# Optimization experiments

Hardware: AMD Instinct MI355X
Metric: run time of the kernel (lower is better)

Reference implementation:

```python
import jax, jax.numpy as jnp
import numpy as np


def _deg2_idx(cpg):
    # pairs (c1, c2) with c1 <= c2, c2 inner loop -> matches torch nested loop order
    i, j = np.triu_indices(cpg)
    return i, j


def _deg3_idx(cpg):
    # triples (c1, c2, c3) with c1 <= c2 <= c3, same nesting order as torch loops
    t = np.array([(a, b, c) for a in range(cpg) for b in range(a, cpg) for c in range(b, cpg)], dtype=np.int32)
    return t[:, 0], t[:, 1], t[:, 2]


def setup_inputs() -> dict:
    key = jax.random.key(0)
    ks = jax.random.split(key, 7)
    B, C, H, W = 16, 256, 56, 56
    G = 32
    cpg = C // G  # 8
    n2 = cpg * (cpg + 1) // 2  # 36
    n3 = sum((i + 1) * (i + 2) // 2 for i in range(cpg))  # 120
    x = jax.random.normal(ks[0], (B, C, H, W), dtype=jnp.float32)
    w1 = jax.random.normal(ks[1], (G, cpg, cpg), dtype=jnp.float32) * 0.1
    b1 = jax.random.normal(ks[2], (G, cpg), dtype=jnp.float32) * 0.1
    w2 = jax.random.normal(ks[3], (G, cpg, n2), dtype=jnp.float32) * 0.1
    b2 = jax.random.normal(ks[4], (G, cpg), dtype=jnp.float32) * 0.1
    w3 = jax.random.normal(ks[5], (G, cpg, n3), dtype=jnp.float32) * 0.1
    b3 = jax.random.normal(ks[6], (G, cpg), dtype=jnp.float32) * 0.1
    return {"x": x, "w1": w1, "b1": b1, "w2": w2, "b2": b2, "w3": w3, "b3": b3}


def reference(x, w1, b1, w2, b2, w3, b3):
    B, C, H, W = x.shape
    G, cpg, _ = w1.shape
    xg = x.reshape(B, G, cpg, H, W)  # [B, G, cpg, H, W]

    i2, j2 = _deg2_idx(cpg)
    a3, b3i, c3 = _deg3_idx(cpg)

    # polynomial feature expansion (per group, vectorized over all dims)
    d2 = xg[:, :, i2] * xg[:, :, j2]                        # [B, G, n2, H, W]
    d3 = xg[:, :, a3] * xg[:, :, b3i] * xg[:, :, c3]        # [B, G, n3, H, W]

    # grouped 1x1 convs as per-group matmuls, summed (matches output += conv(...))
    out = jnp.einsum('bgkhw,gok->bgohw', xg, w1) + b1[None, :, :, None, None]
    out = out + jnp.einsum('bgkhw,gok->bgohw', d2, w2) + b2[None, :, :, None, None]
    out = out + jnp.einsum('bgkhw,gok->bgohw', d3, w3) + b3[None, :, :, None, None]
    return out.reshape(B, C, H, W)
```

## Files before the change

kernel.cpp:

```cpp
#include <hip/hip_runtime.h>

#define CPG 8
#define NGRP 32
#define NB 16
#define HW 3136
#define HU 784
#define N2 36
#define N3 120
#define NF 165
#define WSTRIDE (NF * CPG)

typedef float vfloat4 __attribute__((ext_vector_type(4)));

__host__ __device__ constexpr int idx2(int i, int j) {
    return i * CPG - i * (i - 1) / 2 + (j - i);
}
__host__ __device__ constexpr int idx3(int a, int b, int c) {
    int base = 0;
    for (int t = 0; t < a; ++t) { int m = CPG - t; base += m * (m + 1) / 2; }
    for (int t = a; t < b; ++t) base += CPG - t;
    return base + (c - b);
}

__device__ inline vfloat4 splat4(float s) { return (vfloat4){s, s, s, s}; }

__global__ __launch_bounds__(256) void prep_weights(
    const float* __restrict__ w1, const float* __restrict__ b1,
    const float* __restrict__ w2, const float* __restrict__ b2,
    const float* __restrict__ w3, const float* __restrict__ b3,
    float* __restrict__ ws)
{
    const int g = blockIdx.x;
    for (int idx = threadIdx.x; idx < WSTRIDE; idx += 256) {
        const int f = idx >> 3, o = idx & 7;
        const int ch = g * CPG + o;
        float v;
        if (f < 8)        v = w1[ch * CPG + f];
        else if (f < 44)  v = w2[ch * N2 + (f - 8)];
        else if (f < 164) v = w3[ch * N3 + (f - 44)];
        else              v = b1[ch] + b2[ch] + b3[ch];
        ws[g * WSTRIDE + idx] = v;
    }
}

#define ACCUMS(F, T) do {                                                    \
    const float w0 = wp[(F) * 8 + 0], w1_ = wp[(F) * 8 + 1];                 \
    const float w2_ = wp[(F) * 8 + 2], w3_ = wp[(F) * 8 + 3];                \
    const float w4_ = wp[(F) * 8 + 4], w5_ = wp[(F) * 8 + 5];                \
    const float w6_ = wp[(F) * 8 + 6], w7_ = wp[(F) * 8 + 7];                \
    acc[0] += w0  * (T); acc[1] += w1_ * (T);                                \
    acc[2] += w2_ * (T); acc[3] += w3_ * (T);                                \
    acc[4] += w4_ * (T); acc[5] += w5_ * (T);                                \
    acc[6] += w6_ * (T); acc[7] += w7_ * (T);                                \
} while (0)

__global__ __launch_bounds__(256, 2) void hoaf_sload(
    const float* __restrict__ x,
    const float* __restrict__ ws,
    float* __restrict__ out)
{
    const int tid   = threadIdx.x;
    const int g     = blockIdx.x;
    const int b     = blockIdx.y;
    const int chunk = blockIdx.z;

    const int q = tid + chunk * 256;
    if (q >= HU) return;

    const float* __restrict__ wp = ws + g * WSTRIDE;

    const size_t base = ((size_t)(b * NGRP + g) * CPG) * HW;
    const vfloat4* x4 = (const vfloat4*)(x + base);
    vfloat4*       o4 = (vfloat4*)(out + base);

    vfloat4 xv[CPG];
#pragma unroll
    for (int c = 0; c < CPG; ++c) xv[c] = x4[(size_t)c * HU + q];

    vfloat4 acc[CPG];
#pragma unroll
    for (int o = 0; o < CPG; ++o) acc[o] = splat4(wp[164 * 8 + o]);

#pragma unroll
    for (int k = 0; k < CPG; ++k) ACCUMS(k, xv[k]);

#pragma unroll
    for (int i = 0; i < CPG; ++i) {
#pragma unroll
        for (int j = i; j < CPG; ++j) {
            const vfloat4 p = xv[i] * xv[j];
            ACCUMS(8 + idx2(i, j), p);
#pragma unroll
            for (int a = 0; a <= i; ++a) {
                const vfloat4 t = xv[a] * p;
                ACCUMS(44 + idx3(a, i, j), t);
            }
        }
    }

#pragma unroll
    for (int o = 0; o < CPG; ++o) o4[(size_t)o * HU + q] = acc[o];
}

#define ACCUM(F, T) do {                                                       \
    const vfloat4 wa = *reinterpret_cast<const vfloat4*>(&wt[(F)][0]);         \
    const vfloat4 wb = *reinterpret_cast<const vfloat4*>(&wt[(F)][4]);         \
    acc[0] += wa.x * (T); acc[1] += wa.y * (T);                                \
    acc[2] += wa.z * (T); acc[3] += wa.w * (T);                                \
    acc[4] += wb.x * (T); acc[5] += wb.y * (T);                                \
    acc[6] += wb.z * (T); acc[7] += wb.w * (T);                                \
} while (0)
#define FENCE() __builtin_amdgcn_sched_barrier(0)

__global__ __launch_bounds__(256, 4) void hoaf_lds(
    const float* __restrict__ x,
    const float* __restrict__ w1, const float* __restrict__ b1,
    const float* __restrict__ w2, const float* __restrict__ b2,
    const float* __restrict__ w3, const float* __restrict__ b3,
    float* __restrict__ out)
{
    __shared__ __align__(16) float wt[165][8];

    const int tid   = threadIdx.x;
    const int g     = blockIdx.x;
    const int b     = blockIdx.y;
    const int chunk = blockIdx.z;

    for (int idx = tid; idx < 165 * 8; idx += 256) {
        const int f = idx >> 3, o = idx & 7;
        const int ch = g * CPG + o;
        float v;
        if (f < 8)        v = w1[ch * CPG + f];
        else if (f < 44)  v = w2[ch * N2 + (f - 8)];
        else if (f < 164) v = w3[ch * N3 + (f - 44)];
        else              v = b1[ch] + b2[ch] + b3[ch];
        wt[f][o] = v;
    }
    __syncthreads();

    const int q = tid + chunk * 256;
    if (q >= HU) return;

    const vfloat4 b_lo = *reinterpret_cast<const vfloat4*>(&wt[164][0]);
    const vfloat4 b_hi = *reinterpret_cast<const vfloat4*>(&wt[164][4]);

    const size_t base = ((size_t)(b * NGRP + g) * CPG) * HW;
    const vfloat4* x4 = (const vfloat4*)(x + base);
    vfloat4*       o4 = (vfloat4*)(out + base);

    vfloat4 xv[CPG];
#pragma unroll
    for (int c = 0; c < CPG; ++c) xv[c] = x4[(size_t)c * HU + q];

    vfloat4 acc[CPG];
    acc[0] = splat4(b_lo.x); acc[1] = splat4(b_lo.y);
    acc[2] = splat4(b_lo.z); acc[3] = splat4(b_lo.w);
    acc[4] = splat4(b_hi.x); acc[5] = splat4(b_hi.y);
    acc[6] = splat4(b_hi.z); acc[7] = splat4(b_hi.w);

#pragma unroll
    for (int k = 0; k < CPG; k += 2) {
        ACCUM(k, xv[k]);
        ACCUM(k + 1, xv[k + 1]);
        FENCE();
    }

#pragma unroll
    for (int i = 0; i < CPG; ++i) {
#pragma unroll
        for (int j = i; j < CPG; ++j) {
            const vfloat4 p = xv[i] * xv[j];
            ACCUM(8 + idx2(i, j), p);
#pragma unroll
            for (int a = 0; a <= i; ++a) {
                const vfloat4 t = xv[a] * p;
                ACCUM(44 + idx3(a, i, j), t);
            }
            FENCE();
        }
    }

#pragma unroll
    for (int o = 0; o < CPG; ++o) o4[(size_t)o * HU + q] = acc[o];
}

extern "C" void kernel_launch(void* const* d_in, const int* in_sizes, int n_in,
                              void* d_out, int out_size, void* d_ws, size_t ws_size,
                              hipStream_t stream) {
    const float* x  = (const float*)d_in[0];
    const float* w1 = (const float*)d_in[1];
    const float* b1 = (const float*)d_in[2];
    const float* w2 = (const float*)d_in[3];
    const float* b2 = (const float*)d_in[4];
    const float* w3 = (const float*)d_in[5];
    const float* b3 = (const float*)d_in[6];
    float* out = (float*)d_out;
    float* ws  = (float*)d_ws;

    dim3 grid(NGRP, NB, 4);
    dim3 block(256);

    const size_t ws_needed = (size_t)NGRP * WSTRIDE * sizeof(float);
    if (ws != nullptr && ws_size >= ws_needed) {
        prep_weights<<<dim3(NGRP), dim3(256), 0, stream>>>(w1, b1, w2, b2, w3, b3, ws);
        hoaf_sload<<<grid, block, 0, stream>>>(x, ws, out);
    } else {
        hoaf_lds<<<grid, block, 0, stream>>>(x, w1, b1, w2, b2, w3, b3, out);
    }
}
```

Before: 147.1 us.

## Split output channels across two blocks to cut register pressure

The scalar-load kernel now computes only 4 of the 8 output channels per thread, and the grid's z dimension doubles so a second set of blocks handles the other half. This shrinks the accumulator registers, and the launch bounds become waves_per_eu(2,6) to allow higher occupancy. In exchange, each block recomputes the full set of degree-2 and degree-3 products and reads x twice, roughly doubling the multiply work spent on feature expansion.

```diff
diff --git a/kernel.cpp b/kernel.cpp
--- a/kernel.cpp
+++ b/kernel.cpp
@@ -43,18 +43,16 @@
     }
 }
 
-#define ACCUMS(F, T) do {                                                    \
+#define ACCUMS4(F, T) do {                                                   \
     const float w0 = wp[(F) * 8 + 0], w1_ = wp[(F) * 8 + 1];                 \
     const float w2_ = wp[(F) * 8 + 2], w3_ = wp[(F) * 8 + 3];                \
-    const float w4_ = wp[(F) * 8 + 4], w5_ = wp[(F) * 8 + 5];                \
-    const float w6_ = wp[(F) * 8 + 6], w7_ = wp[(F) * 8 + 7];                \
     acc[0] += w0  * (T); acc[1] += w1_ * (T);                                \
     acc[2] += w2_ * (T); acc[3] += w3_ * (T);                                \
-    acc[4] += w4_ * (T); acc[5] += w5_ * (T);                                \
-    acc[6] += w6_ * (T); acc[7] += w7_ * (T);                                \
 } while (0)
 
-__global__ __launch_bounds__(256, 2) void hoaf_sload(
+__global__ __launch_bounds__(256)
+__attribute__((amdgpu_waves_per_eu(2, 6)))
+void hoaf_sload4(
     const float* __restrict__ x,
     const float* __restrict__ ws,
     float* __restrict__ out)
@@ -62,44 +60,46 @@
     const int tid   = threadIdx.x;
     const int g     = blockIdx.x;
     const int b     = blockIdx.y;
-    const int chunk = blockIdx.z;
+    const int z     = blockIdx.z;
+    const int chunk = z & 3;
+    const int h4    = (z >> 2) * 4;
 
     const int q = tid + chunk * 256;
     if (q >= HU) return;
 
-    const float* __restrict__ wp = ws + g * WSTRIDE;
+    const float* __restrict__ wp = ws + g * WSTRIDE + h4;
 
     const size_t base = ((size_t)(b * NGRP + g) * CPG) * HW;
     const vfloat4* x4 = (const vfloat4*)(x + base);
-    vfloat4*       o4 = (vfloat4*)(out + base);
+    vfloat4*       o4 = (vfloat4*)(out + base) + (size_t)h4 * HU;
 
     vfloat4 xv[CPG];
 #pragma unroll
     for (int c = 0; c < CPG; ++c) xv[c] = x4[(size_t)c * HU + q];
 
-    vfloat4 acc[CPG];
-#pragma unroll
-    for (int o = 0; o < CPG; ++o) acc[o] = splat4(wp[164 * 8 + o]);
-
-#pragma unroll
-    for (int k = 0; k < CPG; ++k) ACCUMS(k, xv[k]);
+    vfloat4 acc[4];
+#pragma unroll
+    for (int o = 0; o < 4; ++o) acc[o] = splat4(wp[164 * 8 + o]);
+
+#pragma unroll
+    for (int k = 0; k < CPG; ++k) ACCUMS4(k, xv[k]);
 
 #pragma unroll
     for (int i = 0; i < CPG; ++i) {
 #pragma unroll
         for (int j = i; j < CPG; ++j) {
             const vfloat4 p = xv[i] * xv[j];
-            ACCUMS(8 + idx2(i, j), p);
+            ACCUMS4(8 + idx2(i, j), p);
 #pragma unroll
             for (int a = 0; a <= i; ++a) {
                 const vfloat4 t = xv[a] * p;
-                ACCUMS(44 + idx3(a, i, j), t);
+                ACCUMS4(44 + idx3(a, i, j), t);
             }
         }
     }
 
 #pragma unroll
-    for (int o = 0; o < CPG; ++o) o4[(size_t)o * HU + q] = acc[o];
+    for (int o = 0; o < 4; ++o) o4[(size_t)o * HU + q] = acc[o];
 }
 
 #define ACCUM(F, T) do {                                                       \
@@ -197,14 +197,13 @@
     float* out = (float*)d_out;
     float* ws  = (float*)d_ws;
 
-    dim3 grid(NGRP, NB, 4);
-    dim3 block(256);
-
     const size_t ws_needed = (size_t)NGRP * WSTRIDE * sizeof(float);
     if (ws != nullptr && ws_size >= ws_needed) {
         prep_weights<<<dim3(NGRP), dim3(256), 0, stream>>>(w1, b1, w2, b2, w3, b3, ws);
-        hoaf_sload<<<grid, block, 0, stream>>>(x, ws, out);
+        dim3 grid(NGRP, NB, 8);
+        hoaf_sload4<<<grid, dim3(256), 0, stream>>>(x, ws, out);
     } else {
-        hoaf_lds<<<grid, block, 0, stream>>>(x, w1, b1, w2, b2, w3, b3, out);
-    }
-}
+        dim3 grid(NGRP, NB, 4);
+        hoaf_lds<<<grid, dim3(256), 0, stream>>>(x, w1, b1, w2, b2, w3, b3, out);
+    }
+}
```

New measurement: 149.5 us. About the same (+1.6%).
